# Kernel optimization log

Hardware: AMD Instinct MI355X
Metric: run time of the kernel (lower is better)

## Reference

```python
import jax, jax.numpy as jnp
import numpy as np

B, NQ, NV, DIM, H, F = 32, 197, 1568, 768, 12, 8


def setup_inputs() -> dict:
    key = jax.random.key(0)
    ks = jax.random.split(key, 5)
    return {
        "x": jax.random.normal(ks[0], (B, NV, DIM), jnp.float32),
        "question": jax.random.normal(ks[1], (B, NQ, DIM), jnp.float32),
        "Wq": jax.random.normal(ks[2], (DIM, DIM), jnp.float32) * 0.02,
        "Wkv": jax.random.normal(ks[3], (DIM, 2 * DIM), jnp.float32) * 0.02,
        "Wproj": jax.random.normal(ks[4], (DIM, DIM), jnp.float32) * 0.02,
        "bproj": jnp.zeros((DIM,), jnp.float32),
        "f": F,
    }


def _heads(t, h):
    # 'b n (h d) -> (b h) n d'
    b, n, dim = t.shape
    d = dim // h
    return t.reshape(b, n, h, d).transpose(0, 2, 1, 3).reshape(b * h, n, d)


def reference(x, question, Wq, Wkv, Wproj, bproj, f):
    b, nv, dim = x.shape
    h = H
    d = dim // h
    scale = d ** -0.5

    q = _heads(question @ Wq, h) * scale          # (bh, nq, d), pre-scaled as in source
    kv = x @ Wkv
    k = _heads(kv[..., :dim], h)                  # (bh, nv, d)
    v = _heads(kv[..., dim:], h)                  # (bh, nv, d)

    cls_q, q_ = q[:, :1], q[:, 1:]                # cls token vs patch queries

    # cls token attends over ALL video tokens
    cls_sim = jnp.einsum('bid,bjd->bij', cls_q, k)
    cls_out = jnp.einsum('bij,bjd->bid', jax.nn.softmax(cls_sim, axis=-1), v)

    # patch queries attend per-frame: k,v 'b (f n) d -> (b f) n d', q_ repeat_interleave(f)
    n = nv // f
    kf = k.reshape(b * h, f, n, d)
    vf = v.reshape(b * h, f, n, d)
    sim = jnp.einsum('bqd,bfkd->bfqk', q_, kf)    # broadcast == repeat_interleave over frames
    out = jnp.einsum('bfqk,bfkd->bfqd', jax.nn.softmax(sim, axis=-1), vf)
    out = out.reshape(b * h, f * (q.shape[1] - 1), d)  # '(b f) n d -> b (f n) d'

    out = jnp.concatenate([cls_out, out], axis=1)  # (bh, 1 + f*(nq-1), d)
    n_out = out.shape[1]
    # '(b h) n d -> b n (h d)'
    out = out.reshape(b, h, n_out, d).transpose(0, 2, 1, 3).reshape(b, n_out, dim)
    return out @ Wproj + bproj
```

## Files before the change

### kernel.cpp

```cpp
#include <hip/hip_runtime.h>

typedef __bf16 bf16;
typedef __bf16 bf16x8 __attribute__((ext_vector_type(8)));
typedef __bf16 bf16x4 __attribute__((ext_vector_type(4)));
typedef __bf16 bf16x2 __attribute__((ext_vector_type(2)));
typedef float f32x4 __attribute__((ext_vector_type(4)));
typedef float f32x16 __attribute__((ext_vector_type(16)));
typedef unsigned int u32x4 __attribute__((ext_vector_type(4)));

#define MFMA16(a, b, c) __builtin_amdgcn_mfma_f32_16x16x32_bf16(a, b, c, 0, 0, 0)
#define MFMA32(a, b, c) __builtin_amdgcn_mfma_f32_32x32x16_bf16(a, b, c, 0, 0, 0)

__device__ __forceinline__ void gload_lds16(const bf16* g, bf16* l) {
  __builtin_amdgcn_global_load_lds(
      (const __attribute__((address_space(1))) void*)g,
      (__attribute__((address_space(3))) void*)l, 16, 0, 0);
}

__device__ __forceinline__ unsigned pk2(float a, float b) {
  bf16x2 t;
  t[0] = (bf16)a;
  t[1] = (bf16)b;
  return __builtin_bit_cast(unsigned, t);
}

__global__ __launch_bounds__(256) void f2b_k(const float* __restrict__ src,
                                             bf16* __restrict__ dst,
                                             long long n) {
  long long i = ((long long)blockIdx.x * 256 + threadIdx.x) * 8;
  if (i >= n) return;
  const float4 a = *(const float4*)(src + i);
  const float4 b = *(const float4*)(src + i + 4);
  bf16x8 v;
  v[0] = (bf16)a.x; v[1] = (bf16)a.y; v[2] = (bf16)a.z; v[3] = (bf16)a.w;
  v[4] = (bf16)b.x; v[5] = (bf16)b.y; v[6] = (bf16)b.z; v[7] = (bf16)b.w;
  *(bf16x8*)(dst + i) = v;
}

__global__ __launch_bounds__(256) void wconv_k(const float* __restrict__ W,
                                               bf16* __restrict__ Wt,
                                               int K, int N) {
  long long idx = (long long)blockIdx.x * 256 + threadIdx.x;
  if (idx >= (long long)K * N) return;
  int k = (int)(idx % K);
  int n = (int)(idx / K);
  Wt[idx] = (bf16)W[(long long)k * N + n];
}

__global__ __launch_bounds__(256) void transv_k(const bf16* __restrict__ Vb,
                                                bf16* __restrict__ Vt) {
  long long idx = (long long)blockIdx.x * 256 + threadIdx.x;
  const long long total = (long long)384 * 8 * 64 * 224;
  if (idx >= total) return;
  int k = (int)(idx % 224);
  long long t = idx / 224;
  int d = (int)(t % 64);
  t /= 64;
  int fr = (int)(t % 8);
  int bh = (int)(t / 8);
  bf16 v = (bf16)0.0f;
  if (k < 196) v = Vb[((long long)bh * 1568 + fr * 196 + k) * 64 + d];
  Vt[idx] = v;
}

template <int MODE>
__global__ __launch_bounds__(256) void gemm_k(const bf16* __restrict__ A,
                                              const bf16* __restrict__ Bt,
                                              void* __restrict__ Cptr,
                                              bf16* __restrict__ C2,
                                              const float* __restrict__ bias,
                                              int M, int N, int K) {
  __shared__ bf16 As[128 * 64];
  __shared__ bf16 Bs[128 * 64];
  const int tid = threadIdx.x;
  const int lane = tid & 63, w = tid >> 6;
  const int wm = w & 1, wn = w >> 1;
  const int col = lane & 15, quad = lane >> 4;
  const int m0 = blockIdx.x * 128, n0 = blockIdx.y * 128;

  const int rsub = lane >> 3;
  const int segg = (lane & 7) ^ rsub;
  const bf16* Ag0 = A + (long long)(m0 + w * 32 + rsub) * K + segg * 8;
  const bf16* Bg0 = Bt + (long long)(n0 + w * 32 + rsub) * K + segg * 8;
  bf16* Al0 = As + (w * 32) * 64;
  bf16* Bl0 = Bs + (w * 32) * 64;

  f32x4 acc[4][4] = {};
  const int sA = col & 7;

  for (int k0 = 0; k0 < K; k0 += 64) {
    __syncthreads();
#pragma unroll
    for (int j = 0; j < 4; ++j)
      gload_lds16(Ag0 + (long long)j * 8 * K + k0, Al0 + j * 8 * 64);
#pragma unroll
    for (int j = 0; j < 4; ++j)
      gload_lds16(Bg0 + (long long)j * 8 * K + k0, Bl0 + j * 8 * 64);
    __syncthreads();

#pragma unroll
    for (int kk2 = 0; kk2 < 2; ++kk2) {
      const int s = kk2 * 4 + quad;
      const int slot = (s ^ sA) * 8;
      bf16x8 af[4], bfr[4];
#pragma unroll
      for (int mt = 0; mt < 4; ++mt)
        af[mt] = *(const bf16x8*)&As[(wm * 64 + mt * 16 + col) * 64 + slot];
#pragma unroll
      for (int nt = 0; nt < 4; ++nt)
        bfr[nt] = *(const bf16x8*)&Bs[(wn * 64 + nt * 16 + col) * 64 + slot];
#pragma unroll
      for (int mt = 0; mt < 4; ++mt) {
#pragma unroll
        for (int nt = 0; nt < 4; ++nt)
          acc[mt][nt] = MFMA16(af[mt], bfr[nt], acc[mt][nt]);
      }
    }
  }

#pragma unroll
  for (int mt = 0; mt < 4; ++mt) {
#pragma unroll
    for (int nt = 0; nt < 4; ++nt) {
      const int gn = n0 + wn * 64 + nt * 16 + col;
      float bv = 0.f;
      if (MODE == 2) bv = bias[gn];
#pragma unroll
      for (int r = 0; r < 4; ++r) {
        const int gm = m0 + wm * 64 + mt * 16 + quad * 4 + r;
        if (gm >= M) continue;
        const float v = acc[mt][nt][r];
        if (MODE == 0) {
          ((bf16*)Cptr)[(long long)gm * N + gn] = (bf16)(v * 0.125f);
        } else if (MODE == 1) {
          const int b = gm / 1568, j = gm - b * 1568;
          if (gn < 768) {
            const int hh = gn >> 6, dd = gn & 63;
            ((bf16*)Cptr)[((long long)(b * 12 + hh) * 1568 + j) * 64 + dd] = (bf16)v;
          } else {
            const int g2 = gn - 768;
            const int hh = g2 >> 6, dd = g2 & 63;
            C2[((long long)(b * 12 + hh) * 1568 + j) * 64 + dd] = (bf16)v;
          }
        } else {
          ((float*)Cptr)[(long long)gm * N + gn] = v + bv;
        }
      }
    }
  }
}

__global__ __launch_bounds__(256) void attn_k(const bf16* __restrict__ qs,
                                              const bf16* __restrict__ Kb,
                                              const bf16* __restrict__ Vt,
                                              bf16* __restrict__ Ob) {
  __shared__ bf16 Ks[224 * 64];
  const int bh = blockIdx.x, fr = blockIdx.y;
  const int b = bh / 12, h = bh % 12;
  const int tid = threadIdx.x, lane = tid & 63, w = tid >> 6;
  const int col = lane & 31, half = lane >> 5;
  const bf16* Qb = qs + (long long)b * 197 * 768 + h * 64;
  const bf16* Kbase = Kb + ((long long)bh * 1568 + fr * 196) * 64;
  const bf16* Vbase = Vt + (long long)(bh * 8 + fr) * 64 * 224;

  {
    const int rsub = lane >> 3;
    const int segg = (lane & 7) ^ rsub;
    const bf16* g0 = Kbase + (long long)(w * 56 + rsub) * 64 + segg * 8;
    bf16* l0 = Ks + (w * 56) * 64;
#pragma unroll
    for (int j = 0; j < 7; ++j)
      gload_lds16(g0 + (long long)j * 8 * 64, l0 + j * 8 * 64);
  }
  __syncthreads();

  for (int mt = w; mt < 7; mt += 4) {
    const int qq = mt * 32 + col;
    const int tok = (qq < 196) ? qq + 1 : 196;
    const bf16* qp = Qb + (long long)tok * 768 + half * 8;
    bf16x8 qf[4];
#pragma unroll
    for (int t = 0; t < 4; ++t) qf[t] = *(const bf16x8*)(qp + 16 * t);

    f32x16 o0 = {}, o1 = {};
    float m = -1e30f, l = 0.f;

#pragma unroll 2
    for (int nt = 0; nt < 7; ++nt) {
      bf16x8 vf[4];
#pragma unroll
      for (int wdw = 0; wdw < 2; ++wdw)
#pragma unroll
        for (int dt = 0; dt < 2; ++dt)
          vf[wdw * 2 + dt] = *(const bf16x8*)(Vbase +
              (long long)(dt * 32 + col) * 224 + nt * 32 + wdw * 16 + half * 8);

      f32x16 s = {};
#pragma unroll
      for (int t = 0; t < 4; ++t) {
        const int row = nt * 32 + col;
        const int sgm = 2 * t + half;
        const bf16x8 kf =
            *(const bf16x8*)&Ks[row * 64 + ((sgm ^ (row & 7)) << 3)];
        s = MFMA32(kf, qf[t], s);
      }
      if (nt == 6) {
#pragma unroll
        for (int r = 0; r < 16; ++r) {
          if (r >= 4) s[r] = -1e30f;
          else if (half) s[r] = -1e30f;
        }
      }

      float tm = s[0];
#pragma unroll
      for (int r = 1; r < 16; ++r) tm = fmaxf(tm, s[r]);
      tm = fmaxf(tm, __shfl_xor(tm, 32, 64));

      if (__any(tm > m + 8.f)) {
        const float mn = fmaxf(m, tm);
        const float sc = __expf(m - mn);
        l *= sc;
#pragma unroll
        for (int r = 0; r < 16; ++r) {
          const float scr = __shfl(sc, (r & 3) + 8 * (r >> 2) + 4 * half, 64);
          o0[r] *= scr;
          o1[r] *= scr;
        }
        m = mn;
      }

      float ls = 0.f;
#pragma unroll
      for (int r = 0; r < 16; ++r) {
        s[r] = __expf(s[r] - m);
        ls += s[r];
      }
      l += ls;
      unsigned pk[8];
#pragma unroll
      for (int i = 0; i < 8; ++i) pk[i] = pk2(s[2 * i], s[2 * i + 1]);

#pragma unroll
      for (int wdw = 0; wdw < 2; ++wdw) {
        const unsigned xa = half ? pk[4 * wdw + 0] : pk[4 * wdw + 2];
        const unsigned xb = half ? pk[4 * wdw + 1] : pk[4 * wdw + 3];
        const unsigned ya = __shfl_xor(xa, 32, 64);
        const unsigned yb = __shfl_xor(xb, 32, 64);
        const unsigned oa = half ? pk[4 * wdw + 2] : pk[4 * wdw + 0];
        const unsigned ob = half ? pk[4 * wdw + 3] : pk[4 * wdw + 1];
        u32x4 wv;
        wv[0] = half ? ya : oa;
        wv[1] = half ? yb : ob;
        wv[2] = half ? oa : ya;
        wv[3] = half ? ob : yb;
        const bf16x8 pa = __builtin_bit_cast(bf16x8, wv);
        o0 = MFMA32(pa, vf[wdw * 2 + 0], o0);
        o1 = MFMA32(pa, vf[wdw * 2 + 1], o1);
      }
    }

    const float lt = l + __shfl_xor(l, 32, 64);
    const float inv = 1.f / lt;
#pragma unroll
    for (int r = 0; r < 16; ++r) {
      const int qr = (r & 3) + 8 * (r >> 2) + 4 * half;
      const float invr = __shfl(inv, qr, 64);
      const int q2 = mt * 32 + qr;
      if (q2 < 196) {
        const int token = 1 + fr * 196 + q2;
        bf16* op = Ob + ((long long)b * 1569 + token) * 768 + h * 64 + col;
        op[0] = (bf16)(o0[r] * invr);
        op[32] = (bf16)(o1[r] * invr);
      }
    }
  }
}

__global__ __launch_bounds__(256) void cls_k(const bf16* __restrict__ qs,
                                             const bf16* __restrict__ Kb,
                                             const bf16* __restrict__ Vt,
                                             bf16* __restrict__ Ob) {
  __shared__ float qsm[64];
  __shared__ float ssm[1568];
  __shared__ float red[256];
  __shared__ float osm[4][64];
  const int bh = blockIdx.x;
  const int b = bh / 12, h = bh % 12;
  const int tid = threadIdx.x;
  if (tid < 64) qsm[tid] = (float)qs[(long long)b * 197 * 768 + h * 64 + tid];
  __syncthreads();

  float lmax = -1e30f;
  for (int j = tid; j < 1568; j += 256) {
    const bf16* kp = Kb + ((long long)bh * 1568 + j) * 64;
    float s = 0.f;
#pragma unroll
    for (int seg = 0; seg < 8; ++seg) {
      const bf16x8 kv = *(const bf16x8*)(kp + seg * 8);
#pragma unroll
      for (int i = 0; i < 8; ++i) s += qsm[seg * 8 + i] * (float)kv[i];
    }
    ssm[j] = s;
    lmax = fmaxf(lmax, s);
  }
  red[tid] = lmax;
  __syncthreads();
  for (int sft = 128; sft > 0; sft >>= 1) {
    if (tid < sft) red[tid] = fmaxf(red[tid], red[tid + sft]);
    __syncthreads();
  }
  const float mx = red[0];
  __syncthreads();

  float lsum = 0.f;
  for (int j = tid; j < 1568; j += 256) {
    const float p = __expf(ssm[j] - mx);
    ssm[j] = p;
    lsum += p;
  }
  red[tid] = lsum;
  __syncthreads();
  for (int sft = 128; sft > 0; sft >>= 1) {
    if (tid < sft) red[tid] += red[tid + sft];
    __syncthreads();
  }
  const float inv = 1.f / red[0];
  __syncthreads();

  const int d = tid & 63, c = tid >> 6;
  float acc = 0.f;
  for (int fr = c * 2; fr < c * 2 + 2; ++fr) {
    const bf16* vp = Vt + ((long long)(bh * 8 + fr) * 64 + d) * 224;
    const float* pp = &ssm[fr * 196];
    for (int k = 0; k < 196; ++k) acc += pp[k] * (float)vp[k];
  }
  osm[c][d] = acc;
  __syncthreads();
  if (tid < 64) {
    const float o = (osm[0][tid] + osm[1][tid] + osm[2][tid] + osm[3][tid]) * inv;
    Ob[(long long)b * 1569 * 768 + h * 64 + tid] = (bf16)o;
  }
}

extern "C" void kernel_launch(void* const* d_in, const int* in_sizes, int n_in,
                              void* d_out, int out_size, void* d_ws, size_t ws_size,
                              hipStream_t stream) {
  const float* x        = (const float*)d_in[0];
  const float* question = (const float*)d_in[1];
  const float* Wq       = (const float*)d_in[2];
  const float* Wkv      = (const float*)d_in[3];
  const float* Wproj    = (const float*)d_in[4];
  const float* bproj    = (const float*)d_in[5];
  float* out = (float*)d_out;

  char* wsb = (char*)d_ws;
  const long long SZ_WQT  = 768LL * 768 * 2;
  const long long SZ_WKVT = 1536LL * 768 * 2;
  const long long SZ_WPT  = 768LL * 768 * 2;
  const long long SZ_QNB  = 32LL * 197 * 768 * 2;
  const long long SZ_Q    = 32LL * 197 * 768 * 2;
  const long long SZ_K    = 384LL * 1568 * 64 * 2;
  const long long SZ_VO   = 50208LL * 768 * 2;

  long long off = 0;
  bf16* Wqt  = (bf16*)(wsb + off); off += SZ_WQT;
  bf16* Wkvt = (bf16*)(wsb + off); off += SZ_WKVT;
  bf16* Wpt  = (bf16*)(wsb + off); off += SZ_WPT;
  bf16* qnb  = (bf16*)(wsb + off); off += SZ_QNB;
  bf16* qsb  = (bf16*)(wsb + off); off += SZ_Q;
  bf16* Kb   = (bf16*)(wsb + off); off += SZ_K;
  bf16* Vb   = (bf16*)(wsb + off); off += SZ_VO;
  bf16* Ob   = Vb;
  bf16* xb   = (bf16*)(wsb + off);
  bf16* Vt   = (bf16*)(wsb + off);

  const long long nx = 32LL * 1568 * 768;
  const long long nq = 32LL * 197 * 768;
  f2b_k<<<(int)((nx / 8 + 255) / 256), 256, 0, stream>>>(x, xb, nx);
  f2b_k<<<(int)((nq / 8 + 255) / 256), 256, 0, stream>>>(question, qnb, nq);

  wconv_k<<<(768 * 768) / 256, 256, 0, stream>>>(Wq, Wqt, 768, 768);
  wconv_k<<<(768 * 1536) / 256, 256, 0, stream>>>(Wkv, Wkvt, 768, 1536);
  wconv_k<<<(768 * 768) / 256, 256, 0, stream>>>(Wproj, Wpt, 768, 768);

  gemm_k<0><<<dim3(50, 6), 256, 0, stream>>>(qnb, Wqt, qsb, nullptr, nullptr,
                                             6304, 768, 768);
  gemm_k<1><<<dim3(392, 12), 256, 0, stream>>>(xb, Wkvt, Kb, Vb, nullptr,
                                               50176, 1536, 768);
  transv_k<<<(384 * 8 * 64 * 224) / 256, 256, 0, stream>>>(Vb, Vt);

  cls_k<<<384, 256, 0, stream>>>(qsb, Kb, Vt, Ob);
  attn_k<<<dim3(384, 8), 256, 0, stream>>>(qsb, Kb, Vt, Ob);

  gemm_k<2><<<dim3(393, 6), 256, 0, stream>>>(Ob, Wpt, out, nullptr, bproj,
                                              50208, 768, 768);
}
```

Before: 908.1 us.

## Fuse V transpose into KV GEMM epilogue and add 256x256 double-buffered GEMM

Drops the separate V transpose and padding kernel. The KV projection epilogue now writes V straight into the per-frame transposed, padded layout that attention reads, and a small kernel zeroes only the pad columns. The KV and output-projection GEMMs move to a new 256x256-tile, 512-thread kernel with double-buffered LDS and an XCD-aware block-to-tile remapping. The aim is to cut a full extra pass over V through memory and to raise GEMM data reuse. The cost is a large LDS footprint per block, which lowers occupancy, plus more workspace reshuffling.

```diff
diff --git a/kernel.cpp b/kernel.cpp
--- a/kernel.cpp
+++ b/kernel.cpp
@@ -47,27 +47,22 @@
   Wt[idx] = (bf16)W[(long long)k * N + n];
 }
 
-__global__ __launch_bounds__(256) void transv_k(const bf16* __restrict__ Vb,
-                                                bf16* __restrict__ Vt) {
+__global__ __launch_bounds__(256) void pad0_k(bf16* __restrict__ Vt) {
   long long idx = (long long)blockIdx.x * 256 + threadIdx.x;
-  const long long total = (long long)384 * 8 * 64 * 224;
+  const long long total = 3072LL * 64 * 7;
   if (idx >= total) return;
-  int k = (int)(idx % 224);
-  long long t = idx / 224;
+  int c = (int)(idx % 7);
+  long long t = idx / 7;
   int d = (int)(t % 64);
-  t /= 64;
-  int fr = (int)(t % 8);
-  int bh = (int)(t / 8);
-  bf16 v = (bf16)0.0f;
-  if (k < 196) v = Vb[((long long)bh * 1568 + fr * 196 + k) * 64 + d];
-  Vt[idx] = v;
+  long long f = t / 64;
+  bf16x4 z = {};
+  *(bf16x4*)&Vt[(f * 64 + d) * 224 + 196 + c * 4] = z;
 }
 
 template <int MODE>
 __global__ __launch_bounds__(256) void gemm_k(const bf16* __restrict__ A,
                                               const bf16* __restrict__ Bt,
                                               void* __restrict__ Cptr,
-                                              bf16* __restrict__ C2,
                                               const float* __restrict__ bias,
                                               int M, int N, int K) {
   __shared__ bf16 As[128 * 64];
@@ -123,27 +118,126 @@
 #pragma unroll
     for (int nt = 0; nt < 4; ++nt) {
       const int gn = n0 + wn * 64 + nt * 16 + col;
-      float bv = 0.f;
-      if (MODE == 2) bv = bias[gn];
 #pragma unroll
       for (int r = 0; r < 4; ++r) {
         const int gm = m0 + wm * 64 + mt * 16 + quad * 4 + r;
         if (gm >= M) continue;
         const float v = acc[mt][nt][r];
-        if (MODE == 0) {
-          ((bf16*)Cptr)[(long long)gm * N + gn] = (bf16)(v * 0.125f);
-        } else if (MODE == 1) {
-          const int b = gm / 1568, j = gm - b * 1568;
-          if (gn < 768) {
-            const int hh = gn >> 6, dd = gn & 63;
-            ((bf16*)Cptr)[((long long)(b * 12 + hh) * 1568 + j) * 64 + dd] = (bf16)v;
-          } else {
-            const int g2 = gn - 768;
-            const int hh = g2 >> 6, dd = g2 & 63;
-            C2[((long long)(b * 12 + hh) * 1568 + j) * 64 + dd] = (bf16)v;
-          }
+        ((bf16*)Cptr)[(long long)gm * N + gn] = (bf16)(v * 0.125f);
+      }
+    }
+  }
+}
+
+template <int MODE>
+__global__ __launch_bounds__(512) void gemm256_k(
+    const bf16* __restrict__ A, const bf16* __restrict__ Bt,
+    void* __restrict__ Cptr, bf16* __restrict__ C2,
+    const float* __restrict__ bias, int M, int N, int K,
+    int NB, int qq, int rq) {
+  __shared__ bf16 As[2][256 * 64];
+  __shared__ bf16 Bs[2][256 * 64];
+  const int tid = threadIdx.x;
+  const int lane = tid & 63, w = tid >> 6;
+  const int wm = w & 1, wn = w >> 1;
+  const int col = lane & 15, quad = lane >> 4;
+
+  const int bid = blockIdx.x;
+  const int xcd = bid & 7, ii = bid >> 3;
+  const int wg = (xcd < rq ? xcd * (qq + 1) : rq * (qq + 1) + (xcd - rq) * qq) + ii;
+  const int mb = wg / NB, nb = wg - mb * NB;
+  const int m0 = mb * 256, n0 = nb * 256;
+
+  const int rsub = lane >> 3;
+  const int segg = (lane & 7) ^ rsub;
+  const bf16* Ag0 = A + (long long)(m0 + w * 32 + rsub) * K + segg * 8;
+  const bf16* Bg0 = Bt + (long long)(n0 + w * 32 + rsub) * K + segg * 8;
+  const int lbase = (w * 32) * 64;
+
+  f32x4 acc[8][4] = {};
+  const int sA = col & 7;
+
+#pragma unroll
+  for (int j = 0; j < 4; ++j) {
+    gload_lds16(Ag0 + (long long)j * 8 * K, &As[0][lbase + j * 8 * 64]);
+    gload_lds16(Bg0 + (long long)j * 8 * K, &Bs[0][lbase + j * 8 * 64]);
+  }
+  __syncthreads();
+
+  for (int k0 = 0; k0 < K; k0 += 64) {
+    const int cur = (k0 >> 6) & 1;
+    if (k0 + 64 < K) {
+#pragma unroll
+      for (int j = 0; j < 4; ++j) {
+        gload_lds16(Ag0 + (long long)j * 8 * K + k0 + 64,
+                    &As[cur ^ 1][lbase + j * 8 * 64]);
+        gload_lds16(Bg0 + (long long)j * 8 * K + k0 + 64,
+                    &Bs[cur ^ 1][lbase + j * 8 * 64]);
+      }
+    }
+#pragma unroll
+    for (int kk2 = 0; kk2 < 2; ++kk2) {
+      const int slot = ((kk2 * 4 + quad) ^ sA) << 3;
+      bf16x8 af[8], bfv[4];
+#pragma unroll
+      for (int mt = 0; mt < 8; ++mt)
+        af[mt] = *(const bf16x8*)&As[cur][(wm * 128 + mt * 16 + col) * 64 + slot];
+#pragma unroll
+      for (int nt = 0; nt < 4; ++nt)
+        bfv[nt] = *(const bf16x8*)&Bs[cur][(wn * 64 + nt * 16 + col) * 64 + slot];
+#pragma unroll
+      for (int mt = 0; mt < 8; ++mt) {
+#pragma unroll
+        for (int nt = 0; nt < 4; ++nt)
+          acc[mt][nt] = MFMA16(af[mt], bfv[nt], acc[mt][nt]);
+      }
+    }
+    __syncthreads();
+  }
+
+  if (MODE == 1) {
+    bf16* Kbp = (bf16*)Cptr;
+#pragma unroll
+    for (int mt = 0; mt < 8; ++mt) {
+      const int gm0 = m0 + wm * 128 + mt * 16 + quad * 4;
+      if (gm0 >= M) continue;
+      const int bb = gm0 / 1568;
+      const int j0 = gm0 - bb * 1568;
+      const int fr = j0 / 196;
+      const int kk0 = j0 - fr * 196;
+#pragma unroll
+      for (int nt = 0; nt < 4; ++nt) {
+        const int gn = n0 + wn * 64 + nt * 16 + col;
+        if (gn < 768) {
+          const int hh = gn >> 6, dd = gn & 63;
+          bf16* kp = Kbp + ((long long)(bb * 12 + hh) * 1568 + j0) * 64 + dd;
+#pragma unroll
+          for (int r = 0; r < 4; ++r) kp[r * 64] = (bf16)acc[mt][nt][r];
         } else {
-          ((float*)Cptr)[(long long)gm * N + gn] = v + bv;
+          const int g2 = gn - 768;
+          const int hh = g2 >> 6, dd = g2 & 63;
+          bf16x4 pv;
+          pv[0] = (bf16)acc[mt][nt][0];
+          pv[1] = (bf16)acc[mt][nt][1];
+          pv[2] = (bf16)acc[mt][nt][2];
+          pv[3] = (bf16)acc[mt][nt][3];
+          *(bf16x4*)&C2[(((long long)(bb * 12 + hh) * 8 + fr) * 64 + dd) * 224 +
+                        kk0] = pv;
+        }
+      }
+    }
+  } else {
+#pragma unroll
+    for (int mt = 0; mt < 8; ++mt) {
+#pragma unroll
+      for (int nt = 0; nt < 4; ++nt) {
+        const int gn = n0 + wn * 64 + nt * 16 + col;
+        const float bv = bias[gn];
+#pragma unroll
+        for (int r = 0; r < 4; ++r) {
+          const int gm = m0 + wm * 128 + mt * 16 + quad * 4 + r;
+          if (gm < M)
+            ((float*)Cptr)[(long long)gm * N + gn] = acc[mt][nt][r] + bv;
         }
       }
     }
@@ -360,8 +454,8 @@
   const long long SZ_WPT  = 768LL * 768 * 2;
   const long long SZ_QNB  = 32LL * 197 * 768 * 2;
   const long long SZ_Q    = 32LL * 197 * 768 * 2;
+  const long long SZ_XO   = 50208LL * 768 * 2;
   const long long SZ_K    = 384LL * 1568 * 64 * 2;
-  const long long SZ_VO   = 50208LL * 768 * 2;
 
   long long off = 0;
   bf16* Wqt  = (bf16*)(wsb + off); off += SZ_WQT;
@@ -369,10 +463,10 @@
   bf16* Wpt  = (bf16*)(wsb + off); off += SZ_WPT;
   bf16* qnb  = (bf16*)(wsb + off); off += SZ_QNB;
   bf16* qsb  = (bf16*)(wsb + off); off += SZ_Q;
+  bf16* xb   = (bf16*)(wsb + off);
+  bf16* Ob   = xb;
+  off += SZ_XO;
   bf16* Kb   = (bf16*)(wsb + off); off += SZ_K;
-  bf16* Vb   = (bf16*)(wsb + off); off += SZ_VO;
-  bf16* Ob   = Vb;
-  bf16* xb   = (bf16*)(wsb + off);
   bf16* Vt   = (bf16*)(wsb + off);
 
   const long long nx = 32LL * 1568 * 768;
@@ -383,16 +477,16 @@
   wconv_k<<<(768 * 768) / 256, 256, 0, stream>>>(Wq, Wqt, 768, 768);
   wconv_k<<<(768 * 1536) / 256, 256, 0, stream>>>(Wkv, Wkvt, 768, 1536);
   wconv_k<<<(768 * 768) / 256, 256, 0, stream>>>(Wproj, Wpt, 768, 768);
-
-  gemm_k<0><<<dim3(50, 6), 256, 0, stream>>>(qnb, Wqt, qsb, nullptr, nullptr,
+  pad0_k<<<(3072 * 64 * 7) / 256, 256, 0, stream>>>(Vt);
+
+  gemm_k<0><<<dim3(50, 6), 256, 0, stream>>>(qnb, Wqt, qsb, nullptr,
                                              6304, 768, 768);
-  gemm_k<1><<<dim3(392, 12), 256, 0, stream>>>(xb, Wkvt, Kb, Vb, nullptr,
-                                               50176, 1536, 768);
-  transv_k<<<(384 * 8 * 64 * 224) / 256, 256, 0, stream>>>(Vb, Vt);
+  gemm256_k<1><<<1176, 512, 0, stream>>>(xb, Wkvt, Kb, Vt, nullptr,
+                                         50176, 1536, 768, 6, 147, 0);
 
   cls_k<<<384, 256, 0, stream>>>(qsb, Kb, Vt, Ob);
   attn_k<<<dim3(384, 8), 256, 0, stream>>>(qsb, Kb, Vt, Ob);
 
-  gemm_k<2><<<dim3(393, 6), 256, 0, stream>>>(Ob, Wpt, out, nullptr, bproj,
-                                              50208, 768, 768);
-}
+  gemm256_k<2><<<591, 512, 0, stream>>>(Ob, Wpt, out, nullptr, bproj,
+                                        50208, 768, 768, 3, 73, 7);
+}
```

After: 816.9 us. 1.11x faster.
